# Kernel optimization log

Measured on AMD Instinct MI355X. Metric: run time of the kernel, lower is better.

The kernel has to match this reference:

```python
import jax, jax.numpy as jnp
import numpy as np

EPS = 1e-12


def _l2norm(x, axis):
    return x / jnp.maximum(jnp.linalg.norm(x, axis=axis, keepdims=True), EPS)


def _wn_weight(v, g):
    # weight norm over input axis (kernel_size=1): W = g * v / ||v||
    return g * v / jnp.maximum(jnp.linalg.norm(v, axis=0, keepdims=True), EPS)


def setup_inputs() -> dict:
    key = jax.random.key(0)
    ks = jax.random.split(key, 8)
    B, T, D = 16, 4096, 512
    N, K, d = 9, 1024, 8
    return {
        "z": jax.random.normal(ks[0], (B, T, D), dtype=jnp.float32),
        "in_v": jax.random.normal(ks[1], (N, D, d), dtype=jnp.float32) * 0.05,
        "in_g": jax.random.uniform(ks[2], (N, d), dtype=jnp.float32) + 0.5,
        "in_b": jax.random.normal(ks[3], (N, d), dtype=jnp.float32) * 0.01,
        "out_v": jax.random.normal(ks[4], (N, d, D), dtype=jnp.float32) * 0.05,
        "out_g": jax.random.uniform(ks[5], (N, D), dtype=jnp.float32) + 0.5,
        "out_b": jax.random.normal(ks[6], (N, D), dtype=jnp.float32) * 0.01,
        "codebooks": jax.random.normal(ks[7], (N, K, d), dtype=jnp.float32),
    }


def reference(z, in_v, in_g, in_b, out_v, out_g, out_b, codebooks):
    # Eval-mode ResidualVectorQuantize: n_quantizers = n_codebooks, mask all True.
    n_codebooks = codebooks.shape[0]
    residual = z
    z_q = jnp.zeros_like(z)
    commitment_loss = jnp.zeros((), z.dtype)
    codebook_loss = jnp.zeros((), z.dtype)
    codes, latents = [], []
    for i in range(n_codebooks):
        # in_proj (weight-normalized 1x1 conv == linear): [B,T,D] -> [B,T,d]
        W_in = _wn_weight(in_v[i], in_g[i])
        z_e = jnp.einsum("btd,dc->btc", residual, W_in) + in_b[i]
        # decode_latents: l2-normalize, pairwise sq-dist, nearest neighbor
        cb = codebooks[i]                      # [K, d] raw codebook
        enc_n = _l2norm(z_e, axis=-1)          # [B, T, d]
        cb_n = _l2norm(cb, axis=-1)            # [K, d]
        dist = (jnp.sum(enc_n * enc_n, -1, keepdims=True)
                - 2.0 * jnp.einsum("btc,kc->btk", enc_n, cb_n)
                + jnp.sum(cb_n * cb_n, -1))    # [B, T, K]
        indices = jnp.argmax(-dist, axis=-1)   # [B, T]
        z_q_i = cb[indices]                    # gather from raw codebook [B,T,d]
        # per-batch losses (mean over T, d)
        commit_i = jnp.mean((z_e - jax.lax.stop_gradient(z_q_i)) ** 2, axis=(1, 2))
        cbloss_i = jnp.mean((z_q_i - jax.lax.stop_gradient(z_e)) ** 2, axis=(1, 2))
        # straight-through estimator
        z_q_st = z_e + jax.lax.stop_gradient(z_q_i - z_e)
        # out_proj: [B,T,d] -> [B,T,D]
        W_out = _wn_weight(out_v[i], out_g[i])
        z_q_proj = jnp.einsum("btc,cd->btd", z_q_st, W_out) + out_b[i]
        z_q = z_q + z_q_proj
        residual = residual - z_q_proj
        commitment_loss = commitment_loss + commit_i.mean()
        codebook_loss = codebook_loss + cbloss_i.mean()
        codes.append(indices)
        latents.append(z_e)
    codes = jnp.stack(codes, axis=2)           # [B, T, N]
    latents = jnp.concatenate(latents, axis=2) # [B, T, N*d]
    return z_q, codes, latents, commitment_loss, codebook_loss
```

## Files before the change

kernel.cpp:

```cpp
#include <hip/hip_runtime.h>
#include <math.h>

#define ROWS   65536

#define WS_WPAD 0
#define WS_WOUT 49152
#define WS_CBT  86016
#define WS_SC   159744
#define WS_M    168960
#define WS_CACC 174144
#define WS_SOB  174216
#define WS_LOSS 174728

#define OUT_CODES 33554432
#define OUT_LAT   34144256
#define OUT_CLOSS 38862848
#define OUT_CBLOSS 38862849

#define SM_AST   0
#define SM_BS    4224
#define SM_P     0
#define SM_QLT   0
#define SM_REG2  9216
#define SM_CODES 18720
#define SM_WARR  19872

__device__ __forceinline__ int pcol(int cc){ return (cc/9)*12 + (cc%9); }

__global__ __launch_bounds__(256) void prep1(const float* __restrict__ in_v,
    const float* __restrict__ in_g, const float* __restrict__ out_v,
    const float* __restrict__ out_g, const float* __restrict__ out_b,
    const float* __restrict__ cb, float* __restrict__ ws)
{
    int t = blockIdx.x*256 + threadIdx.x;
    if (t < 9216) {
        int i = t >> 10, k = t & 1023;
        const float* p = cb + (i*1024 + k)*8;
        float v[8]; float ssq = 0.f;
        #pragma unroll
        for (int c=0;c<8;c++){ v[c]=p[c]; ssq = fmaf(v[c],v[c],ssq); }
        float den = fmaxf(sqrtf(ssq), 1e-12f);
        float sc = 0.f;
        #pragma unroll
        for (int c=0;c<8;c++){ float cn = v[c]/den; ws[WS_CBT + (i*8+c)*1024 + k] = cn; sc = fmaf(cn,cn,sc); }
        ws[WS_SC + i*1024 + k] = sc;
    } else if (t < 13824) {
        int r = t - 9216; int j = r >> 9, tt = r & 511;
        float v[8]; float ssq = 0.f;
        #pragma unroll
        for (int a=0;a<8;a++){ v[a]=out_v[(j*8+a)*512+tt]; ssq=fmaf(v[a],v[a],ssq); }
        float den = fmaxf(sqrtf(ssq), 1e-12f);
        float g = out_g[j*512+tt];
        #pragma unroll
        for (int a=0;a<8;a++) ws[WS_WOUT + (j*8+a)*512 + tt] = g*v[a]/den;
    } else if (t < 18432) {
        int r = t - 13824;
        int w = r >> 6, l = r & 63;
        int i = w >> 3, c = w & 7;
        float v[8]; float ssq = 0.f;
        #pragma unroll
        for (int u=0;u<8;u++){ v[u] = in_v[(i*512 + l*8+u)*8 + c]; ssq = fmaf(v[u],v[u],ssq); }
        #pragma unroll
        for (int off=1; off<64; off<<=1) ssq += __shfl_xor(ssq, off, 64);
        float den = fmaxf(sqrtf(ssq), 1e-12f);
        float g = in_g[i*8+c];
        int pc = pcol(i*8+c);
        #pragma unroll
        for (int u=0;u<8;u++) ws[WS_WPAD + (l*8+u)*96 + pc] = g*v[u]/den;
    } else if (t < 18944) {
        int tt = t - 18432;
        float s = 0.f;
        for (int j=0;j<9;j++) s += out_b[j*512+tt];
        ws[WS_SOB + tt] = s;
    } else if (t == 18944) {
        *(double*)&ws[WS_LOSS] = 0.0;
    }
}

__global__ __launch_bounds__(256) void prep2(const float* __restrict__ out_b,
                                             float* __restrict__ ws)
{
    int g = blockIdx.x*256 + threadIdx.x;
    if (g < 41472) {
        int oi = g >> 3, part = g & 7;
        int j = oi / 576; int rem = oi % 576; int i = rem >> 6; int ab = rem & 63;
        int a = ab >> 3, b = ab & 7;
        int pc = pcol(i*8+b);
        const float* wo = ws + WS_WOUT + (j*8+a)*512 + part*64;
        const float* wp = ws + WS_WPAD + (part*64)*96 + pc;
        float s = 0.f;
        #pragma unroll
        for (int u=0; u<16; u++) {
            float4 w4 = *(const float4*)(wo + u*4);
            s = fmaf(w4.x, wp[(u*4+0)*96], s);
            s = fmaf(w4.y, wp[(u*4+1)*96], s);
            s = fmaf(w4.z, wp[(u*4+2)*96], s);
            s = fmaf(w4.w, wp[(u*4+3)*96], s);
        }
        #pragma unroll
        for (int off=1; off<8; off<<=1) s += __shfl_xor(s, off, 64);
        if (part == 0) ws[WS_M + oi] = s;
    } else if (g < 42048) {
        int r = g - 41472;
        int oi = r >> 3, part = r & 7;
        int i = oi >> 3, b = oi & 7;
        int pc = pcol(i*8+b);
        float s = 0.f;
        for (int u=0; u<64; u++) {
            int tt = part*64 + u;
            float bb = 0.f;
            for (int j=0;j<i;j++) bb += out_b[j*512+tt];
            s = fmaf(bb, ws[WS_WPAD + tt*96+pc], s);
        }
        #pragma unroll
        for (int off=1; off<8; off<<=1) s += __shfl_xor(s, off, 64);
        if (part == 0) ws[WS_CACC + oi] = s;
    }
}

__global__ __launch_bounds__(256, 2) void fused_all(
    const float* __restrict__ z, const float* __restrict__ in_b,
    const float* __restrict__ cbooks, float* __restrict__ ws, float* __restrict__ out)
{
    __shared__ __align__(16) float smem[19880];
    int tid = threadIdx.x;
    int brow = blockIdx.x * 128;

    {
        float* AsT = smem + SM_AST;
        float* Bs  = smem + SM_BS;
        int tr = tid & 31, tc = tid >> 5;
        float acc[4][9];
        #pragma unroll
        for (int r=0;r<4;r++){
            #pragma unroll
            for(int c=0;c<9;c++) acc[r][c]=0.f;
        }
        int kq = tid & 7, rr = tid >> 3;
        for (int kk=0; kk<16; kk++) {
            #pragma unroll
            for (int p=0;p<4;p++){
                int row = rr + p*32;
                float4 a = *(const float4*)(z + (size_t)(brow+row)*512 + kk*32 + kq*4);
                AsT[(kq*4+0)*132 + row] = a.x;
                AsT[(kq*4+1)*132 + row] = a.y;
                AsT[(kq*4+2)*132 + row] = a.z;
                AsT[(kq*4+3)*132 + row] = a.w;
            }
            #pragma unroll
            for (int p=0;p<3;p++){
                int idx = p*256 + tid;
                *(float4*)(Bs + idx*4) = *(const float4*)(ws + WS_WPAD + kk*32*96 + idx*4);
            }
            __syncthreads();
            #pragma unroll 4
            for (int k=0;k<32;k++){
                float4 a  = *(const float4*)(AsT + k*132 + tr*4);
                float4 b0 = *(const float4*)(Bs + k*96 + tc*12);
                float4 b1 = *(const float4*)(Bs + k*96 + tc*12 + 4);
                float  b8 = Bs[k*96 + tc*12 + 8];
                float av[4] = {a.x,a.y,a.z,a.w};
                float bv[9] = {b0.x,b0.y,b0.z,b0.w,b1.x,b1.y,b1.z,b1.w,b8};
                #pragma unroll
                for (int r=0;r<4;r++){
                    #pragma unroll
                    for (int c=0;c<9;c++) acc[r][c] = fmaf(av[r], bv[c], acc[r][c]);
                }
            }
            __syncthreads();
        }
        float* P = smem + SM_P;
        #pragma unroll
        for (int c=0;c<9;c++){
            int cc = tc*9+c;
            float bias = in_b[cc];
            #pragma unroll
            for (int r=0;r<4;r++){
                int rl = tr*4 + r;
                P[rl*72 + cc] = acc[r][c] + bias;
            }
        }
        __syncthreads();
    }

    int w  = tid >> 6;
    int l  = tid & 63;
    int rowhalf = l >> 1;
    int ah = l & 1;
    int wrow = brow + w*32;
    int kb = l*16;
    float* P = smem + SM_P;
    float* zen_w = smem + SM_REG2 + w*384;
    float* codes_lds = smem + SM_CODES;

    float lacc = 0.f;
    float4 cbr[4][8];
    float4 hs4[4];

    #pragma unroll 1
    for (int i=0; i<9; i++){
        #pragma unroll
        for (int q=0;q<4;q++){
            #pragma unroll
            for (int c=0;c<8;c++)
                cbr[q][c] = *(const float4*)(ws + WS_CBT + i*8192 + c*1024 + kb + q*4);
            float4 s = *(const float4*)(ws + WS_SC + i*1024 + kb + q*4);
            hs4[q].x = s.x * -0.5f; hs4[q].y = s.y * -0.5f;
            hs4[q].z = s.z * -0.5f; hs4[q].w = s.w * -0.5f;
        }

        int row = wrow + rowhalf;
        int rib = w*32 + rowhalf;
        float* lat = out + OUT_LAT + (size_t)row*72 + i*8;
        float4 p0 = *(const float4*)(P + rib*72 + i*8);
        float4 p1 = *(const float4*)(P + rib*72 + i*8 + 4);
        float ze[8] = {p0.x,p0.y,p0.z,p0.w,p1.x,p1.y,p1.z,p1.w};
        #pragma unroll
        for (int b=0;b<8;b++) ze[b] -= ws[WS_CACC + i*8 + b];
        #pragma unroll 1
        for (int j=0;j<i;j++){
            int kj = (int)codes_lds[rib*9 + j];
            const float* qp = cbooks + (size_t)(j*1024+kj)*8;
            float4 q0 = *(const float4*)(qp);
            float4 q1 = *(const float4*)(qp+4);
            float qa[8] = {q0.x,q0.y,q0.z,q0.w,q1.x,q1.y,q1.z,q1.w};
            const float* M = ws + WS_M + (j*9+i)*64;
            #pragma unroll
            for (int a=0;a<8;a++){
                #pragma unroll
                for (int b=0;b<8;b++) ze[b] = fmaf(-qa[a], M[a*8+b], ze[b]);
            }
        }
        float ssq = 0.f;
        #pragma unroll
        for (int c=0;c<8;c++) ssq = fmaf(ze[c],ze[c],ssq);
        float den = fmaxf(sqrtf(ssq), 1e-12f);
        float rden = 1.0f/den;
        float zen[8];
        #pragma unroll
        for (int c=0;c<8;c++) zen[c] = ze[c]*rden;
        if (ah == 0){
            float4 n0 = {zen[0],zen[1],zen[2],zen[3]};
            float4 n1 = {zen[4],zen[5],zen[6],zen[7]};
            *(float4*)(zen_w + rowhalf*12)     = n0;
            *(float4*)(zen_w + rowhalf*12 + 4) = n1;
        } else {
            float4 z0 = {ze[0],ze[1],ze[2],ze[3]};
            float4 z1 = {ze[4],ze[5],ze[6],ze[7]};
            *(float4*)(lat)   = z0;
            *(float4*)(lat+4) = z1;
        }

        int ksave = 0;
        #pragma unroll 2
        for (int rr=0; rr<32; rr++){
            float4 zv0 = *(const float4*)(zen_w + rr*12);
            float4 zv1 = *(const float4*)(zen_w + rr*12 + 4);
            float zr[8] = {zv0.x,zv0.y,zv0.z,zv0.w,zv1.x,zv1.y,zv1.z,zv1.w};
            float bv = -3.0e38f; int rel = 0;
            #pragma unroll
            for (int q=0;q<4;q++){
                float d0 = hs4[q].x, d1 = hs4[q].y, d2 = hs4[q].z, d3 = hs4[q].w;
                #pragma unroll
                for (int c=0;c<8;c++){
                    d0 = fmaf(zr[c], cbr[q][c].x, d0);
                    d1 = fmaf(zr[c], cbr[q][c].y, d1);
                    d2 = fmaf(zr[c], cbr[q][c].z, d2);
                    d3 = fmaf(zr[c], cbr[q][c].w, d3);
                }
                bool c0 = d0 > bv; rel = c0 ? (q*4+0) : rel; bv = c0 ? d0 : bv;
                bool c1 = d1 > bv; rel = c1 ? (q*4+1) : rel; bv = c1 ? d1 : bv;
                bool c2 = d2 > bv; rel = c2 ? (q*4+2) : rel; bv = c2 ? d2 : bv;
                bool c3 = d3 > bv; rel = c3 ? (q*4+3) : rel; bv = c3 ? d3 : bv;
            }
            int kfull = kb + rel;
            float wm = bv;
            #pragma unroll
            for (int off=1; off<64; off<<=1) wm = fmaxf(wm, __shfl_xor(wm, off, 64));
            unsigned long long msk = __ballot(bv == wm);
            int ln = __ffsll((long long)msk) - 1;
            int kwin = __shfl(kfull, ln, 64);
            ksave = (rowhalf == rr) ? kwin : ksave;
        }

        if (ah == 0){
            const float* qp = cbooks + (size_t)(i*1024+ksave)*8;
            float4 q0 = *(const float4*)(qp);
            float4 q1 = *(const float4*)(qp+4);
            float e0 = ze[0]-q0.x, e1 = ze[1]-q0.y, e2 = ze[2]-q0.z, e3 = ze[3]-q0.w;
            float e4 = ze[4]-q1.x, e5 = ze[5]-q1.y, e6 = ze[6]-q1.z, e7 = ze[7]-q1.w;
            lacc = fmaf(e0,e0,lacc); lacc = fmaf(e1,e1,lacc);
            lacc = fmaf(e2,e2,lacc); lacc = fmaf(e3,e3,lacc);
            lacc = fmaf(e4,e4,lacc); lacc = fmaf(e5,e5,lacc);
            lacc = fmaf(e6,e6,lacc); lacc = fmaf(e7,e7,lacc);
        } else {
            out[OUT_CODES + (size_t)row*9 + i] = (float)ksave;
            codes_lds[rib*9 + i] = (float)ksave;
        }
    }

    {
        float* warr = smem + SM_WARR;
        #pragma unroll
        for (int off=1; off<64; off<<=1) lacc += __shfl_xor(lacc, off, 64);
        if ((tid & 63)==0) warr[w] = lacc;
        __syncthreads();
        if (tid==0){
            double bs = (double)warr[0]+(double)warr[1]+(double)warr[2]+(double)warr[3];
            atomicAdd((double*)&ws[WS_LOSS], bs);
        }
    }

    __syncthreads();
    {
        float* QLT = smem + SM_QLT;
        float* Ws  = smem + SM_REG2;
        if (tid < 128){
            for (int j=0;j<9;j++){
                int kj = (int)codes_lds[tid*9 + j];
                const float* qp = cbooks + (size_t)(j*1024+kj)*8;
                float4 q0 = *(const float4*)qp;
                float4 q1 = *(const float4*)(qp+4);
                QLT[(j*8+0)*128 + tid] = q0.x;
                QLT[(j*8+1)*128 + tid] = q0.y;
                QLT[(j*8+2)*128 + tid] = q0.z;
                QLT[(j*8+3)*128 + tid] = q0.w;
                QLT[(j*8+4)*128 + tid] = q1.x;
                QLT[(j*8+5)*128 + tid] = q1.y;
                QLT[(j*8+6)*128 + tid] = q1.z;
                QLT[(j*8+7)*128 + tid] = q1.w;
            }
        }
        int tc = tid & 15, tr = tid >> 4;
        int aoff = tr*8;
        int boff = tc*8 + (tc>>3)*4;
        for (int cc=0; cc<4; cc++){
            __syncthreads();
            #pragma unroll
            for (int p=0;p<9;p++){
                int idx = p*256 + tid;
                int jr = idx >> 5; int cq = idx & 31;
                float4 wv = *(const float4*)(ws + WS_WOUT + jr*512 + cc*128 + cq*4);
                *(float4*)(Ws + jr*132 + cq*4 + (cq>>4)*4) = wv;
            }
            __syncthreads();
            float acc[8][8];
            #pragma unroll
            for (int r=0;r<8;r++){
                #pragma unroll
                for (int c=0;c<8;c++) acc[r][c]=0.f;
            }
            #pragma unroll 2
            for (int k=0;k<72;k++){
                float4 a0 = *(const float4*)(QLT + k*128 + aoff);
                float4 a1 = *(const float4*)(QLT + k*128 + aoff + 4);
                float4 b0 = *(const float4*)(Ws + k*132 + boff);
                float4 b1 = *(const float4*)(Ws + k*132 + boff + 4);
                float av[8] = {a0.x,a0.y,a0.z,a0.w,a1.x,a1.y,a1.z,a1.w};
                float bw[8] = {b0.x,b0.y,b0.z,b0.w,b1.x,b1.y,b1.z,b1.w};
                #pragma unroll
                for (int r=0;r<8;r++){
                    #pragma unroll
                    for (int c=0;c<8;c++) acc[r][c] = fmaf(av[r], bw[c], acc[r][c]);
                }
            }
            float4 s0 = *(const float4*)(ws + WS_SOB + cc*128 + tc*8);
            float4 s1 = *(const float4*)(ws + WS_SOB + cc*128 + tc*8 + 4);
            #pragma unroll
            for (int r=0;r<8;r++){
                int row = brow + tr*8 + r;
                float4 o0 = {acc[r][0]+s0.x, acc[r][1]+s0.y, acc[r][2]+s0.z, acc[r][3]+s0.w};
                float4 o1 = {acc[r][4]+s1.x, acc[r][5]+s1.y, acc[r][6]+s1.z, acc[r][7]+s1.w};
                *(float4*)(out + (size_t)row*512 + cc*128 + tc*8)     = o0;
                *(float4*)(out + (size_t)row*512 + cc*128 + tc*8 + 4) = o1;
            }
        }
    }
}

__global__ void finalize(const float* __restrict__ ws, float* __restrict__ out)
{
    if (threadIdx.x == 0){
        double L = *(const double*)(ws + WS_LOSS);
        float lv = (float)(L * (1.0/524288.0));
        out[OUT_CLOSS]  = lv;
        out[OUT_CBLOSS] = lv;
    }
}

extern "C" void kernel_launch(void* const* d_in, const int* in_sizes, int n_in,
                              void* d_out, int out_size, void* d_ws, size_t ws_size,
                              hipStream_t stream) {
    const float* z     = (const float*)d_in[0];
    const float* in_v  = (const float*)d_in[1];
    const float* in_g  = (const float*)d_in[2];
    const float* in_b  = (const float*)d_in[3];
    const float* out_v = (const float*)d_in[4];
    const float* out_g = (const float*)d_in[5];
    const float* out_b = (const float*)d_in[6];
    const float* cb    = (const float*)d_in[7];
    float* out = (float*)d_out;
    float* ws  = (float*)d_ws;

    prep1<<<75, 256, 0, stream>>>(in_v, in_g, out_v, out_g, out_b, cb, ws);
    prep2<<<165, 256, 0, stream>>>(out_b, ws);
    fused_all<<<512, 256, 0, stream>>>(z, in_b, cb, ws, out);
    finalize<<<1, 64, 0, stream>>>(ws, out);
}
```

Before: 596.7 us.

## Split codebook search into two half-passes to cut register pressure; swizzle AsT LDS layout

The nearest-codebook search now holds 8 codewords per lane in registers instead of 16, running two passes over 512-entry halves. The first pass's per-row winners go to LDS and are merged in the second pass, with ties keeping the lower index. This is meant to roughly halve the VGPRs used for the codebook tile so occupancy rises, at the cost of running the wavefront max/ballot reduction twice per row. Separately, the transposed A-tile stores in the in-projection GEMM are permuted so the four scalar LDS writes per float4 spread across banks, and the inner loop reads through the matching permuted index.

```diff
diff --git a/kernel.cpp b/kernel.cpp
--- a/kernel.cpp
+++ b/kernel.cpp
@@ -22,6 +22,7 @@
 #define SM_P     0
 #define SM_QLT   0
 #define SM_REG2  9216
+#define SM_WIN   10752
 #define SM_CODES 18720
 #define SM_WARR  19872
 
@@ -142,10 +143,10 @@
             for (int p=0;p<4;p++){
                 int row = rr + p*32;
                 float4 a = *(const float4*)(z + (size_t)(brow+row)*512 + kk*32 + kq*4);
-                AsT[(kq*4+0)*132 + row] = a.x;
-                AsT[(kq*4+1)*132 + row] = a.y;
-                AsT[(kq*4+2)*132 + row] = a.z;
-                AsT[(kq*4+3)*132 + row] = a.w;
+                AsT[(kq     )*132 + row] = a.x;
+                AsT[(kq +  8)*132 + row] = a.y;
+                AsT[(kq + 16)*132 + row] = a.z;
+                AsT[(kq + 24)*132 + row] = a.w;
             }
             #pragma unroll
             for (int p=0;p<3;p++){
@@ -155,7 +156,8 @@
             __syncthreads();
             #pragma unroll 4
             for (int k=0;k<32;k++){
-                float4 a  = *(const float4*)(AsT + k*132 + tr*4);
+                int sk = ((k&3)<<3) | (k>>2);
+                float4 a  = *(const float4*)(AsT + sk*132 + tr*4);
                 float4 b0 = *(const float4*)(Bs + k*96 + tc*12);
                 float4 b1 = *(const float4*)(Bs + k*96 + tc*12 + 4);
                 float  b8 = Bs[k*96 + tc*12 + 8];
@@ -188,27 +190,15 @@
     int rowhalf = l >> 1;
     int ah = l & 1;
     int wrow = brow + w*32;
-    int kb = l*16;
     float* P = smem + SM_P;
     float* zen_w = smem + SM_REG2 + w*384;
+    float* win_w = smem + SM_WIN + w*64;
     float* codes_lds = smem + SM_CODES;
 
     float lacc = 0.f;
-    float4 cbr[4][8];
-    float4 hs4[4];
 
     #pragma unroll 1
     for (int i=0; i<9; i++){
-        #pragma unroll
-        for (int q=0;q<4;q++){
-            #pragma unroll
-            for (int c=0;c<8;c++)
-                cbr[q][c] = *(const float4*)(ws + WS_CBT + i*8192 + c*1024 + kb + q*4);
-            float4 s = *(const float4*)(ws + WS_SC + i*1024 + kb + q*4);
-            hs4[q].x = s.x * -0.5f; hs4[q].y = s.y * -0.5f;
-            hs4[q].z = s.z * -0.5f; hs4[q].w = s.w * -0.5f;
-        }
-
         int row = wrow + rowhalf;
         int rib = w*32 + rowhalf;
         float* lat = out + OUT_LAT + (size_t)row*72 + i*8;
@@ -252,35 +242,68 @@
         }
 
         int ksave = 0;
-        #pragma unroll 2
-        for (int rr=0; rr<32; rr++){
-            float4 zv0 = *(const float4*)(zen_w + rr*12);
-            float4 zv1 = *(const float4*)(zen_w + rr*12 + 4);
-            float zr[8] = {zv0.x,zv0.y,zv0.z,zv0.w,zv1.x,zv1.y,zv1.z,zv1.w};
-            float bv = -3.0e38f; int rel = 0;
-            #pragma unroll
-            for (int q=0;q<4;q++){
-                float d0 = hs4[q].x, d1 = hs4[q].y, d2 = hs4[q].z, d3 = hs4[q].w;
+        #pragma unroll 1
+        for (int p=0; p<2; p++){
+            int kbp = p*512 + l*8;
+            const float* cbb = ws + WS_CBT + i*8192 + kbp;
+            float4 cbr[2][8];
+            #pragma unroll
+            for (int c=0;c<8;c++){
+                cbr[0][c] = *(const float4*)(cbb + c*1024);
+                cbr[1][c] = *(const float4*)(cbb + c*1024 + 4);
+            }
+            float4 s0 = *(const float4*)(ws + WS_SC + i*1024 + kbp);
+            float4 s1 = *(const float4*)(ws + WS_SC + i*1024 + kbp + 4);
+            float4 hs0, hs1;
+            hs0.x = s0.x*-0.5f; hs0.y = s0.y*-0.5f; hs0.z = s0.z*-0.5f; hs0.w = s0.w*-0.5f;
+            hs1.x = s1.x*-0.5f; hs1.y = s1.y*-0.5f; hs1.z = s1.z*-0.5f; hs1.w = s1.w*-0.5f;
+
+            #pragma unroll 2
+            for (int rr=0; rr<32; rr++){
+                float4 zv0 = *(const float4*)(zen_w + rr*12);
+                float4 zv1 = *(const float4*)(zen_w + rr*12 + 4);
+                float zr[8] = {zv0.x,zv0.y,zv0.z,zv0.w,zv1.x,zv1.y,zv1.z,zv1.w};
+                float d0=hs0.x, d1=hs0.y, d2=hs0.z, d3=hs0.w;
+                float d4=hs1.x, d5=hs1.y, d6=hs1.z, d7=hs1.w;
                 #pragma unroll
                 for (int c=0;c<8;c++){
-                    d0 = fmaf(zr[c], cbr[q][c].x, d0);
-                    d1 = fmaf(zr[c], cbr[q][c].y, d1);
-                    d2 = fmaf(zr[c], cbr[q][c].z, d2);
-                    d3 = fmaf(zr[c], cbr[q][c].w, d3);
+                    d0 = fmaf(zr[c], cbr[0][c].x, d0);
+                    d1 = fmaf(zr[c], cbr[0][c].y, d1);
+                    d2 = fmaf(zr[c], cbr[0][c].z, d2);
+                    d3 = fmaf(zr[c], cbr[0][c].w, d3);
+                    d4 = fmaf(zr[c], cbr[1][c].x, d4);
+                    d5 = fmaf(zr[c], cbr[1][c].y, d5);
+                    d6 = fmaf(zr[c], cbr[1][c].z, d6);
+                    d7 = fmaf(zr[c], cbr[1][c].w, d7);
                 }
-                bool c0 = d0 > bv; rel = c0 ? (q*4+0) : rel; bv = c0 ? d0 : bv;
-                bool c1 = d1 > bv; rel = c1 ? (q*4+1) : rel; bv = c1 ? d1 : bv;
-                bool c2 = d2 > bv; rel = c2 ? (q*4+2) : rel; bv = c2 ? d2 : bv;
-                bool c3 = d3 > bv; rel = c3 ? (q*4+3) : rel; bv = c3 ? d3 : bv;
-            }
-            int kfull = kb + rel;
-            float wm = bv;
-            #pragma unroll
-            for (int off=1; off<64; off<<=1) wm = fmaxf(wm, __shfl_xor(wm, off, 64));
-            unsigned long long msk = __ballot(bv == wm);
-            int ln = __ffsll((long long)msk) - 1;
-            int kwin = __shfl(kfull, ln, 64);
-            ksave = (rowhalf == rr) ? kwin : ksave;
+                float bv = d0; int rel = 0;
+                bool c1 = d1 > bv; rel = c1?1:rel; bv = c1?d1:bv;
+                bool c2 = d2 > bv; rel = c2?2:rel; bv = c2?d2:bv;
+                bool c3 = d3 > bv; rel = c3?3:rel; bv = c3?d3:bv;
+                bool c4 = d4 > bv; rel = c4?4:rel; bv = c4?d4:bv;
+                bool c5 = d5 > bv; rel = c5?5:rel; bv = c5?d5:bv;
+                bool c6 = d6 > bv; rel = c6?6:rel; bv = c6?d6:bv;
+                bool c7 = d7 > bv; rel = c7?7:rel; bv = c7?d7:bv;
+
+                float wm = bv;
+                #pragma unroll
+                for (int off=1; off<64; off<<=1) wm = fmaxf(wm, __shfl_xor(wm, off, 64));
+                unsigned long long msk = __ballot(bv == wm);
+                int ln = __ffsll((long long)msk) - 1;
+                int kwin = __shfl(kbp + rel, ln, 64);
+                if (p == 0){
+                    if (l == 0){
+                        float2 pw = {wm, (float)kwin};
+                        *(float2*)(win_w + rr*2) = pw;
+                    }
+                } else {
+                    float2 pw = *(const float2*)(win_w + rr*2);
+                    bool keepA = (pw.x >= wm);
+                    wm   = keepA ? pw.x : wm;
+                    kwin = keepA ? (int)pw.y : kwin;
+                    ksave = (rowhalf == rr) ? kwin : ksave;
+                }
+            }
         }
 
         if (ah == 0){
```

New measurement: 686.7 us. 1.15x slower.
